# Performance work log

Hardware: AMD Instinct MI355X
Metric: run time of the kernel (lower is better)

Reference implementation:

```python
import jax, jax.numpy as jnp
from jax import lax
import numpy as np

B, FH, FW = 8, 50, 50
STRIDE = 16
SCALES = (8, 16, 32)
RATIOS = (0.5, 1.0, 2.0)
A = len(SCALES) * len(RATIOS)           # 9 anchors per location
G = 20                                   # gt boxes per image
IMG = FW * STRIDE                        # 800
PRE_NMS, POST_NMS, NMS_THR = 2000, 300, 0.7
POS_THR, NEG_THR = 0.7, 0.3
N_SAMPLES, POS_FRAC = 256, 0.5
SIGMA2 = 9.0                             # smooth-L1 sigma^2


def _make_anchors():
    # replicates ProposalLayer._generate_anchors (anchor-type-major ordering)
    xyp = np.arange(STRIDE / 2, FW * STRIDE, STRIDE).astype(int)
    centres = np.array(np.meshgrid(xyp, xyp)).T.reshape(-1, 2).astype(np.float32)
    dims = [[STRIDE * s * np.sqrt(r), STRIDE * s * np.sqrt(1.0 / r)]
            for s in SCALES for r in RATIOS]
    anc = np.concatenate([np.concatenate([centres - 0.5 * np.asarray(d, np.float32),
                                          centres + 0.5 * np.asarray(d, np.float32)], axis=1)
                          for d in dims], axis=0)
    inside = ((anc[:, 0] >= 0) & (anc[:, 1] >= 0) &
              (anc[:, 2] <= FH * STRIDE) & (anc[:, 3] <= FW * STRIDE))
    return anc, np.nonzero(inside)[0]

ANCHORS_NP, INSIDE_IDX = _make_anchors()
N_ANCH = ANCHORS_NP.shape[0]             # 22500 = FH*FW*A


def centrehw(b):
    return jnp.concatenate([(b[..., :2] + b[..., 2:]) * 0.5, b[..., 2:] - b[..., :2]], -1)

def yxcord(b):
    return jnp.concatenate([b[..., :2] - 0.5 * b[..., 2:], b[..., :2] + 0.5 * b[..., 2:]], -1)

def invtargets(d, a):
    return jnp.concatenate([a[..., :2] + d[..., :2] * a[..., 2:],
                            a[..., 2:] * jnp.exp(d[..., 2:])], -1)

def box_targets(g, a):
    return jnp.concatenate([(g[..., :2] - a[..., :2]) / a[..., 2:],
                            jnp.log(g[..., 2:] / a[..., 2:])], -1)

def pairwise_iou(b1, b2):
    # b1 [..., M, 4], b2 [..., N, 4] -> [..., M, N]
    a = b1[..., :, None, :]
    b = b2[..., None, :, :]
    tl = jnp.maximum(a[..., :2], b[..., :2])
    br = jnp.minimum(a[..., 2:], b[..., 2:])
    wh = jnp.clip(br - tl, 0.0)
    inter = wh[..., 0] * wh[..., 1]
    a1 = (a[..., 2] - a[..., 0]) * (a[..., 3] - a[..., 1])
    a2 = (b[..., 2] - b[..., 0]) * (b[..., 3] - b[..., 1])
    return inter / jnp.maximum(a1 + a2 - inter, 1e-8)


def _nms_single(boxes, scores):
    # greedy NMS: pre-NMS top-k, pairwise IoU, sequential suppression
    vals, idx = lax.top_k(scores, PRE_NMS)
    b = boxes[idx]                                 # [PRE, 4] score-descending
    iou = pairwise_iou(b, b)                       # [PRE, PRE]
    ar = jnp.arange(PRE_NMS)

    def step(supp, i):
        supp = supp | ((~supp[i]) & (iou[i] > NMS_THR) & (ar > i))
        return supp, None

    supp, _ = lax.scan(step, jnp.zeros(PRE_NMS, bool), jnp.arange(PRE_NMS))
    kv = jnp.where(supp, -jnp.inf, vals)
    tv, ti = lax.top_k(kv, POST_NMS)
    return b[ti] * jnp.isfinite(tv)[:, None]       # zero-pad if < POST kept


def _randsample(labels, key):
    # deterministic stand-in for torch randperm-based anchor subsampling
    r = jax.random.uniform(key, labels.shape)

    def ranks(mask):
        return jnp.argsort(jnp.argsort(jnp.where(mask, r, 2.0), axis=1), axis=1)

    pos = labels == 1
    neg = labels == 0
    n_pos = jnp.minimum(pos.sum(1), int(N_SAMPLES * POS_FRAC))
    keep_pos = pos & (ranks(pos) < n_pos[:, None])
    n_neg = jnp.minimum(neg.sum(1), N_SAMPLES - n_pos)
    keep_neg = neg & (ranks(neg) < n_neg[:, None])
    return jnp.where(keep_pos, 1, jnp.where(keep_neg, 0, -1)).astype(jnp.int32)


def _forward(pred_boxes, cls_scores, gt_boxes):
    anchors = jnp.asarray(ANCHORS_NP)
    ctrhw_a = centrehw(anchors)                    # [N, 4] (cy, cx, h, w)
    Bn = pred_boxes.shape[0]
    pd = pred_boxes.transpose(0, 2, 3, 1).reshape(Bn, -1, 4)     # [B, N, 4]
    cls2 = cls_scores.transpose(0, 2, 3, 1).reshape(Bn, -1, 2)   # [B, N, 2]
    pos_scores = cls_scores[:, A:].transpose(0, 2, 3, 1).reshape(Bn, -1)

    proposals = jnp.clip(yxcord(invtargets(pd, ctrhw_a[None])), 0.0, IMG - 1.0)
    top = jnp.floor(jax.vmap(_nms_single)(proposals, pos_scores))

    # ---- training losses ----
    iou = pairwise_iou(gt_boxes, anchors[None])    # [B, G, N]
    max_iou = iou.max(axis=1)
    argmax_bbox = jnp.argmax(iou, axis=1)          # best gt per anchor [B, N]
    labels = jnp.full((Bn, N_ANCH), -1, jnp.int32)
    labels = jnp.where(max_iou < NEG_THR, 0, labels)
    labels = jnp.where(max_iou >= POS_THR, 1, labels)
    gt_best = jnp.argmax(iou, axis=2)              # best anchor per gt [B, G]
    labels = labels.at[jnp.arange(Bn)[:, None], gt_best].set(1)
    labels = labels.at[:, INSIDE_IDX].set(-1)      # replicates source exactly as written
    labels = _randsample(labels, jax.random.key(42))

    g = jnp.take_along_axis(gt_boxes, argmax_bbox[:, :, None], axis=1)  # [B, N, 4]
    tgt = box_targets(centrehw(g), ctrhw_a[None])

    mask = labels != -1
    logp = jax.nn.log_softmax(cls2, axis=-1)
    per = -jnp.take_along_axis(logp, jnp.clip(labels, 0, 1)[..., None], axis=-1)[..., 0]
    cls_loss = (per * mask).sum() / jnp.maximum(mask.sum(), 1)

    in_w = (labels == 1).astype(pd.dtype)[..., None]
    out_w = mask.astype(pd.dtype)[..., None] / jnp.maximum((labels[0] >= 0).sum(), 1).astype(pd.dtype)
    d = in_w * (pd - tgt)
    ad = jnp.abs(d)
    l1 = jnp.where(ad < 1.0 / SIGMA2, 0.5 * SIGMA2 * d * d, ad - 0.5 / SIGMA2)
    bbox_loss = (out_w * l1).sum()
    return top, bbox_loss, cls_loss


def setup_inputs():
    key = jax.random.key(0)
    k1, k2, k3, k4 = jax.random.split(key, 4)
    pred_boxes = 0.1 * jax.random.normal(k1, (B, 4 * A, FH, FW), jnp.float32)
    cls_scores = jax.random.normal(k2, (B, 2 * A, FH, FW), jnp.float32)
    tl = jax.random.uniform(k3, (B, G, 2), minval=0.0, maxval=600.0)
    sz = jax.random.uniform(k4, (B, G, 2), minval=16.0, maxval=180.0)
    gt_boxes = jnp.concatenate([tl, jnp.minimum(tl + sz, IMG - 1.0)], axis=-1)
    return {"pred_boxes": pred_boxes, "cls_scores": cls_scores, "gt_boxes": gt_boxes}


def reference(pred_boxes, cls_scores, gt_boxes):
    return _forward(pred_boxes, cls_scores, gt_boxes)
```

## Files before the change

### kernel.cpp

```cpp
#include <hip/hip_runtime.h>
#include <math.h>

typedef unsigned long long u64;
typedef unsigned int u32;

#define BN 8
#define NA_T 9
#define NPOS 2500
#define FHW 50
#define N_ANCH 22500
#define NG 20
#define PRE 2000
#define POST 300
#define TOTAL (BN * N_ANCH)
#define HALF_RNG 90000u
#define NBLK 256
#define NFLAGS 240
#define MAGIC 0x9E3779B97F4A7C15ull

#define SCOPE_AGENT __HIP_MEMORY_SCOPE_AGENT


__device__ __forceinline__ float iou_f(float ax1, float ay1, float ax2, float ay2,
                                       float bx1, float by1, float bx2, float by2) {
    float tlx = fmaxf(ax1, bx1), tly = fmaxf(ay1, by1);
    float brx = fminf(ax2, bx2), bry = fminf(ay2, by2);
    float wx = fmaxf(brx - tlx, 0.0f);
    float wy = fmaxf(bry - tly, 0.0f);
    float inter = wx * wy;
    float a1 = (ax2 - ax1) * (ay2 - ay1);
    float a2 = (bx2 - bx1) * (by2 - by1);
    float den = fmaxf(a1 + a2 - inter, 1e-8f);
    return inter / den;
}

__device__ __forceinline__ unsigned int f32_sort_asc(float f) {
    unsigned int u = __float_as_uint(f);
    return (u & 0x80000000u) ? ~u : (u | 0x80000000u);
}

#define TF_R(r) { x0 += x1; x1 = ((x1 << r) | (x1 >> (32 - r))); x1 ^= x0; }
__device__ __forceinline__ unsigned int threefry_bits(unsigned int j) {
    unsigned int i = (j < HALF_RNG) ? j : j - HALF_RNG;
    unsigned int x0 = i, x1 = i + HALF_RNG;
    const unsigned int ks0 = 0u, ks1 = 42u, ks2 = 0x1BD11BDAu ^ 0u ^ 42u;
    x0 += ks0; x1 += ks1;
    TF_R(13) TF_R(15) TF_R(26) TF_R(6)
    x0 += ks1; x1 += ks2 + 1u;
    TF_R(17) TF_R(29) TF_R(16) TF_R(24)
    x0 += ks2; x1 += ks0 + 2u;
    TF_R(13) TF_R(15) TF_R(26) TF_R(6)
    x0 += ks0; x1 += ks1 + 3u;
    TF_R(17) TF_R(29) TF_R(16) TF_R(24)
    x0 += ks1; x1 += ks2 + 4u;
    TF_R(13) TF_R(15) TF_R(26) TF_R(6)
    x0 += ks2; x1 += ks0 + 5u;
    return (j < HALF_RNG) ? x0 : x1;
}

__device__ __forceinline__ float smooth_l1(float d) {
    float ad = fabsf(d);
    return (ad < (float)(1.0 / 9.0)) ? (4.5f * d) * d : (ad - (float)(0.5 / 9.0));
}

__device__ __forceinline__ u64 shflx64(u64 v, int m) {
    u32 lo = (u32)v, hi = (u32)(v >> 32);
    lo = (u32)__shfl_xor((int)lo, m);
    hi = (u32)__shfl_xor((int)hi, m);
    return (((u64)hi) << 32) | lo;
}

__device__ __forceinline__ u64 aload_rlx(u64* p) {
    return __hip_atomic_load(p, __ATOMIC_RELAXED, SCOPE_AGENT);
}
__device__ __forceinline__ void astore_rlx(u64* p, u64 v) {
    __hip_atomic_store(p, v, __ATOMIC_RELAXED, SCOPE_AGENT);
}
__device__ __forceinline__ void astore_u32(u32* p, u32 v) {
    __hip_atomic_store(p, v, __ATOMIC_RELAXED, SCOPE_AGENT);
}
__device__ __forceinline__ int aload32(int* p) {
    return __hip_atomic_load(p, __ATOMIC_RELAXED, SCOPE_AGENT);
}
__device__ __forceinline__ void astore32(int* p, int v) {
    __hip_atomic_store(p, v, __ATOMIC_RELAXED, SCOPE_AGENT);
}


struct Shm {
    u32 histA[4096];
    u64 poolB[2048];
    u64 sk[2048];
    float4 accb[POST];
    float accbA[POST];
    u64 Smat[64];
    u64 wsup[16];
    u32 s_out[2];
    u32 s_cnt, s_cnt2, s_cnt3;
    int s_scount;
    int sgb[NG];
    u64 sT, sTp, sTn;
    float2 whl[9];
    float4 g2[2 * NG];
    float swv[16];
    int swi[16];
    double rdc[32];
};

__device__ __forceinline__ void init_whl(Shm& S) {
    if (threadIdx.x < 9) {
        const double scl[3] = {8.0, 16.0, 32.0};
        const double rat[3] = {0.5, 1.0, 2.0};
        double s = 16.0 * scl[threadIdx.x / 3];
        double r = rat[threadIdx.x % 3];
        S.whl[threadIdx.x] = make_float2((float)(s * sqrt(r)), (float)(s * sqrt(1.0 / r)));
    }
}

__device__ __forceinline__ u64 block_sum_u64(u64 v, u64* sred, int nwaves) {
    for (int o = 32; o >= 1; o >>= 1) v += __shfl_down(v, o);
    int wid = threadIdx.x >> 6;
    if ((threadIdx.x & 63) == 0) sred[wid] = v;
    __syncthreads();
    u64 s = 0;
    for (int i = 0; i < nwaves; ++i) s += sred[i];
    return s;
}

__device__ __forceinline__ void hist_pick(const u32* hist, int nb,
                                          u32 remaining, u32* s_out) {
    if (threadIdx.x < 64) {
        int lane = threadIdx.x;
        int bpl = nb >> 6;
        int base = lane * bpl;
        u32 s = 0;
        for (int i = 0; i < bpl; ++i) s += hist[base + i];
        u32 p = s;
        for (int o = 1; o < 64; o <<= 1) {
            u32 t = __shfl_up(p, o);
            if (lane >= o) p += t;
        }
        u32 e = p - s;
        if (e < remaining && remaining <= p) {
            u32 cum = e;
            for (int i = 0; i < bpl; ++i) {
                u32 h = hist[base + i];
                if (cum + h >= remaining) {
                    s_out[0] = (u32)(base + i);
                    s_out[1] = remaining - cum;
                    break;
                }
                cum += h;
            }
        }
    }
    __syncthreads();
}

__device__ __forceinline__ int wave_push(u32* ctr, bool pred) {
    u64 m = __ballot(pred);
    if (m == 0) return -1;
    int lane = threadIdx.x & 63;
    int leader = __ffsll((long long)m) - 1;
    u32 base = 0;
    if (lane == leader) base = atomicAdd(ctr, (u32)__popcll(m));
    base = (u32)__shfl((int)base, leader);
    return pred ? (int)(base + __popcll(m & ((1ull << lane) - 1ull))) : -1;
}


__device__ __forceinline__ void topk_nms(Shm& S, const float* cls, const float* pred,
                                         float* out, int b) {
    int tid = threadIdx.x, lane = tid & 63, wid = tid >> 6;
    const float* cb = cls + ((size_t)b * 18 + 9) * NPOS;
    u32* skw = (u32*)S.sk;
    if (tid < 2) S.s_out[tid] = 0;
    for (int i = tid; i < 4096; i += 1024) { S.histA[i] = 0; skw[i] = 0; }
    __syncthreads();
    {
        int cpy = wid & 3;
        u32* H = ((cpy & 2) ? skw : S.histA) + ((cpy & 1) ? 2048 : 0);
        u32 xr = (u32)(cpy << 3);
        for (int i = tid; i < 5625; i += 1024) {
            float4 v = ((const float4*)cb)[i];
            atomicAdd(&H[(((~f32_sort_asc(v.x)) >> 21) ^ xr)], 1u);
            atomicAdd(&H[(((~f32_sort_asc(v.y)) >> 21) ^ xr)], 1u);
            atomicAdd(&H[(((~f32_sort_asc(v.z)) >> 21) ^ xr)], 1u);
            atomicAdd(&H[(((~f32_sort_asc(v.w)) >> 21) ^ xr)], 1u);
        }
    }
    __syncthreads();
    for (int bn = tid; bn < 2048; bn += 1024) {
        u32 s0 = S.histA[bn];
        u32 s1 = S.histA[2048 + (bn ^ 8)];
        u32 s2 = skw[bn ^ 16];
        u32 s3 = skw[2048 + (bn ^ 24)];
        S.histA[bn] = s0 + s1 + s2 + s3;
    }
    __syncthreads();
    hist_pick(S.histA, 2048, PRE, S.s_out);
    u32 d0 = S.s_out[0], r0 = S.s_out[1];
    u32 bincnt = S.histA[d0];
    bool fast = bincnt <= 2048;
    for (int i = tid; i < 2048; i += 1024) S.sk[i] = 0xFFFFFFFFFFFFFFFFull - (u32)i;
    if (tid == 0) { S.s_cnt = 0; S.s_cnt2 = 0; }
    __syncthreads();
    for (int c = 0; c < 22; ++c) {
        int m = tid + c * 1024;
        bool valid = m < N_ANCH;
        u32 kd = valid ? ~f32_sort_asc(cb[m]) : 0xFFFFFFFFu;
        int n = valid ? ((m % NPOS) * 9 + m / NPOS) : 0;
        u64 kk = (((u64)kd) << 15) | (u32)n;
        u32 topb = kd >> 21;
        int ps = wave_push(&S.s_cnt, valid && topb < d0);
        if (ps >= 0) S.sk[ps] = kk;
        int pb = wave_push(&S.s_cnt2, valid && fast && topb == d0);
        if (pb >= 0) S.poolB[pb] = kk;
    }
    __syncthreads();
    int bc = (int)S.s_cnt2;

    u64 T;
    u64 prefix = ((u64)d0) << 36;
    if (fast) {
        for (int i = tid; i < 4096; i += 1024) S.histA[i] = 0;
        __syncthreads();
        u64 himask = ~((1ull << 36) - 1);
        for (int i = tid; i < bc; i += 1024) {
            u64 kk = S.poolB[i];
            if ((kk & himask) == prefix)
                atomicAdd(&S.histA[(u32)((kk >> 24) & 4095ull)], 1u);
        }
        __syncthreads();
        hist_pick(S.histA, 4096, r0, S.s_out);
        u64 prefix2 = prefix | (((u64)S.s_out[0]) << 24);
        u32 rem2 = S.s_out[1];
        __syncthreads();
        u64* subb = (u64*)S.histA;
        if (tid == 0) S.s_cnt3 = 0;
        __syncthreads();
        u64 himask2 = ~((1ull << 24) - 1);
        for (int i = tid; i < bc; i += 1024) {
            u64 kk = S.poolB[i];
            int ps = wave_push(&S.s_cnt3, (kk & himask2) == prefix2);
            if (ps >= 0) subb[ps] = kk;
        }
        __syncthreads();
        int sc = (int)S.s_cnt3;
        for (int i = tid; i < sc; i += 1024) {
            u64 ki = subb[i]; int rank = 0;
            for (int j = 0; j < sc; ++j) rank += (subb[j] < ki);
            if (rank == (int)rem2 - 1) S.sT = ki;
        }
        __syncthreads();
        T = S.sT;
        for (int i = tid; i < bc; i += 1024) {
            u64 kk = S.poolB[i];
            int ps = wave_push(&S.s_cnt, kk <= T);
            if (ps >= 0) S.sk[ps] = kk;
        }
    } else {
        u32 remaining = r0;
        for (int p = 0; p < 3; ++p) {
            int sh = 24 - 12 * p;
            for (int i = tid; i < 4096; i += 1024) S.histA[i] = 0;
            __syncthreads();
            u64 himask = ~((1ull << (sh + 12)) - 1);
            for (int c = 0; c < 22; ++c) {
                int m = tid + c * 1024;
                if (m < N_ANCH) {
                    int n = (m % NPOS) * 9 + m / NPOS;
                    u64 kk = (((u64)(~f32_sort_asc(cb[m]))) << 15) | (u32)n;
                    if ((kk & himask) == prefix)
                        atomicAdd(&S.histA[(u32)((kk >> sh) & 4095ull)], 1u);
                }
            }
            __syncthreads();
            hist_pick(S.histA, 4096, remaining, S.s_out);
            prefix |= ((u64)S.s_out[0]) << sh;
            remaining = S.s_out[1];
            __syncthreads();
        }
        T = prefix;
        for (int c = 0; c < 22; ++c) {
            int m = tid + c * 1024;
            bool valid = m < N_ANCH;
            u32 kd = valid ? ~f32_sort_asc(cb[m]) : 0xFFFFFFFFu;
            int n = valid ? ((m % NPOS) * 9 + m / NPOS) : 0;
            u64 kk = (((u64)kd) << 15) | (u32)n;
            int ps = wave_push(&S.s_cnt, valid && (kd >> 21) == d0 && kk <= T);
            if (ps >= 0) S.sk[ps] = kk;
        }
    }
    __syncthreads();

    {
        int base = wid * 128;
        u64 v0 = S.sk[base + lane];
        u64 v1 = S.sk[base + 64 + lane];
        for (int k = 2; k <= 128; k <<= 1) {
            bool up0 = ((lane & k) == 0);
            bool up1 = (((64 + lane) & k) == 0);
            for (int j = k >> 1; j > 0; j >>= 1) {
                if (j == 64) {
                    u64 lo = v0 < v1 ? v0 : v1;
                    u64 hi = v0 < v1 ? v1 : v0;
                    v0 = lo; v1 = hi;
                } else {
                    u64 p0 = shflx64(v0, j);
                    u64 p1 = shflx64(v1, j);
                    bool lower = ((lane & j) == 0);
                    bool km0 = (lower == up0);
                    bool km1 = (lower == up1);
                    v0 = km0 ? (v0 < p0 ? v0 : p0) : (v0 > p0 ? v0 : p0);
                    v1 = km1 ? (v1 < p1 ? v1 : p1) : (v1 > p1 ? v1 : p1);
                }
            }
        }
        S.sk[base + lane] = v0;
        S.sk[base + 64 + lane] = v1;
    }
    __syncthreads();

    {
        u64* src = S.sk; u64* dst = S.poolB;
        for (int Sz = 128; Sz < 2048; Sz <<= 1) {
            for (int e = 0; e < 2; ++e) {
                int i = tid + e * 1024;
                u64 key = src[i];
                int pairBase = i & ~(2 * Sz - 1);
                int t = i - pairBase;
                const u64* other; int p;
                if (t < Sz) { other = src + pairBase + Sz; p = t; }
                else        { other = src + pairBase;      p = t - Sz; }
                int lo = 0, hi = Sz;
                while (lo < hi) {
                    int mid = (lo + hi) >> 1;
                    if (other[mid] < key) lo = mid + 1; else hi = mid;
                }
                dst[pairBase + p + lo] = key;
            }
            __syncthreads();
            u64* tmp = src; src = dst; dst = tmp;
        }
    }

    float2* bl = (float2*)S.poolB;
    float2* bh = (float2*)S.sk;
    for (int i = tid; i < 2048; i += 1024) {
        float2 lo = make_float2(0.f, 0.f), hi = make_float2(0.f, 0.f);
        if (i < PRE) {
            int n = (int)(S.sk[i] & 0x7fffu);
            int d = n / NPOS, k = n % NPOS;
            float2 wh = S.whl[d];
            float cx = (float)(8 + 16 * (k / FHW));
            float cy = (float)(8 + 16 * (k % FHW));
            float ax1 = cx - 0.5f * wh.x, ay1 = cy - 0.5f * wh.y;
            float ax2 = cx + 0.5f * wh.x, ay2 = cy + 0.5f * wh.y;
            float acx = (ax1 + ax2) * 0.5f, acy = (ay1 + ay2) * 0.5f;
            float aw = ax2 - ax1, ah = ay2 - ay1;
            int a = n % NA_T, hw = n / NA_T;
            const float* pb = pred + (size_t)b * 36 * NPOS;
            float dx = pb[(4 * a + 0) * NPOS + hw];
            float dy = pb[(4 * a + 1) * NPOS + hw];
            float dw = pb[(4 * a + 2) * NPOS + hw];
            float dh = pb[(4 * a + 3) * NPOS + hw];
            float px = acx + dx * aw, py = acy + dy * ah;
            float pw = aw * expf(dw), ph = ah * expf(dh);
            float x1 = px - 0.5f * pw, y1 = py - 0.5f * ph;
            float x2 = px + 0.5f * pw, y2 = py + 0.5f * ph;
            x1 = fminf(fmaxf(x1, 0.0f), 799.0f);
            y1 = fminf(fmaxf(y1, 0.0f), 799.0f);
            x2 = fminf(fmaxf(x2, 0.0f), 799.0f);
            y2 = fminf(fmaxf(y2, 0.0f), 799.0f);
            lo = make_float2(x1, y1); hi = make_float2(x2, y2);
        }
        bl[i] = lo; bh[i] = hi;
    }
    if (tid == 0) S.s_scount = 0;
    __syncthreads();

    for (int c = 0; c < 32; ++c) {
        int A = S.s_scount;
        int base = c * 64;
        float2 clo = bl[base + lane], chi = bh[base + lane];
        float myA = (chi.x - clo.x) * (chi.y - clo.y);
        bool sup = false;
        for (int a = wid; a < A; a += 16) {
            float4 ab = S.accb[a];
            float tlx = fmaxf(ab.x, clo.x), tly = fmaxf(ab.y, clo.y);
            float brx = fminf(ab.z, chi.x), bry = fminf(ab.w, chi.y);
            float wx = fmaxf(brx - tlx, 0.0f), wy = fmaxf(bry - tly, 0.0f);
            float inter = wx * wy;
            float den = fmaxf(S.accbA[a] + myA - inter, 1e-8f);
            sup |= inter > 0.7f * den;
            if (__all(sup)) break;
        }
        u64 bal = __ballot(sup);
        if (lane == 0) S.wsup[wid] = bal;
        #pragma unroll
        for (int q = 0; q < 4; ++q) {
            int o = wid * 4 + q;
            float2 olo = bl[base + o], ohi = bh[base + o];
            float oA = (ohi.x - olo.x) * (ohi.y - olo.y);
            float tlx = fmaxf(olo.x, clo.x), tly = fmaxf(olo.y, clo.y);
            float brx = fminf(ohi.x, chi.x), bry = fminf(ohi.y, chi.y);
            float wx = fmaxf(brx - tlx, 0.0f), wy = fmaxf(bry - tly, 0.0f);
            float inter = wx * wy;
            float den = fmaxf(oA + myA - inter, 1e-8f);
            bool hit = inter > 0.7f * den;
            u64 m = __ballot(hit);
            if (lane == 0) S.Smat[o] = m;
        }
        __syncthreads();
        if (wid == 0) {
            u64 my_smat = S.Smat[lane];
            u32 sm_lo = (u32)my_smat, sm_hi = (u32)(my_smat >> 32);
            u64 supmask = 0;
            #pragma unroll
            for (int i2 = 0; i2 < 16; ++i2) supmask |= S.wsup[i2];
            int jmax = min(64, PRE - base);
            u64 valid = (jmax >= 64) ? ~0ull : ((1ull << jmax) - 1ull);
            u64 live = (~supmask) & valid;
            int count = A;
            u64 accmask = 0;
            while (live && count < POST) {
                int i = __ffsll((long long)live) - 1;
                u32 rlo = (u32)__builtin_amdgcn_readlane((int)sm_lo, i);
                u32 rhi = (u32)__builtin_amdgcn_readlane((int)sm_hi, i);
                u64 sm = (((u64)rhi) << 32) | rlo;
                accmask |= (1ull << i);
                live &= ~sm & ~(1ull << i);
                count++;
            }
            if (accmask & (1ull << lane)) {
                int pos = A + __popcll(accmask & ((1ull << lane) - 1ull));
                S.accb[pos] = make_float4(clo.x, clo.y, chi.x, chi.y);
                S.accbA[pos] = myA;
            }
            if (lane == 0) S.s_scount = count;
        }
        __syncthreads();
        if (S.s_scount >= POST) break;
    }
    int cntk = S.s_scount;
    for (int s = tid; s < POST; s += 1024) {
        float4 v = make_float4(0.f, 0.f, 0.f, 0.f);
        if (s < cntk) {
            float4 p = S.accb[s];
            v = make_float4(floorf(p.x), floorf(p.y), floorf(p.z), floorf(p.w));
        }
        ((float4*)out)[(size_t)b * POST + s] = v;
    }
}


__device__ __forceinline__ void sample_loss(Shm& S, const u32* samp, int* gtb,
                                            const float* pred, const float* cls,
                                            const float* gt, u64* slots, int b) {
    int tid = threadIdx.x, lane = tid & 63, wid = tid >> 6;
    u32* bitmap = (u32*)S.poolB;
    u64* sred   = S.poolB + 512;
    u64* bufN   = S.poolB + 640;
    u32* hP = S.histA;
    u32* hN = S.histA + 2048;
    u64* bufP = S.sk;
    u64* bufNf = S.sk + 1024;
    const u32* sb = samp + (size_t)b * N_ANCH;

    if (tid < 2) S.s_out[tid] = 0;
    for (int i = tid; i < 704; i += 1024) bitmap[i] = 0;
    for (int i = tid; i < 4096; i += 1024) S.histA[i] = 0;
    if (tid < NG) S.sgb[tid] = aload32(&gtb[b * NG + tid]);
    __syncthreads();

    for (int i = tid; i < 5625; i += 1024) {
        uint4 v = ((const uint4*)sb)[i];
        #pragma unroll
        for (int q = 0; q < 4; ++q) {
            u32 sp = (q == 0) ? v.x : (q == 1) ? v.y : (q == 2) ? v.z : v.w;
            int enc = (int)(sp & 3u);
            if (enc == 2) atomicAdd(&hP[sp >> 21], 1u);
            if (enc == 1) atomicAdd(&hN[sp >> 21], 1u);
        }
    }
    if (tid < NG) {
        int gn = S.sgb[tid];
        atomicOr(&bitmap[gn >> 5], 1u << (gn & 31));
    }
    __syncthreads();
    if (tid < NG) {
        int gn = S.sgb[tid];
        bool dup = false;
        for (int j = 0; j < tid; ++j) dup |= (S.sgb[j] == gn);
        if (!dup) {
            u32 sp = sb[(gn % 9) * NPOS + gn / 9];
            int enc = (int)(sp & 3u);
            if (enc != 3) {
                if (enc != 2) atomicAdd(&hP[sp >> 21], 1u);
                if (enc == 1) atomicSub(&hN[sp >> 21], 1u);
            }
        }
    }
    __syncthreads();

    u32 aP = 0, aN = 0;
    for (int i = tid; i < 2048; i += 1024) { aP += hP[i]; aN += hN[i]; }
    u64 packed = block_sum_u64(((u64)aP << 32) | (u64)aN, sred, 16);
    int cpt = (int)(packed >> 32), ctot = (int)(packed & 0xffffffffu);
    int np = min(cpt, 128), nn = min(ctot, 256 - np);

    bool needP = cpt > np, needN = ctot > nn;
    u32 dN = 0, remN = 0;
    if (needN) {
        hist_pick(hN, 2048, (u32)nn, S.s_out);
        dN = S.s_out[0]; remN = S.s_out[1];
        __syncthreads();
    }
    int gN = needN ? (nn - (int)remN + (int)hN[dN]) : ctot;
    bool fastS = (cpt <= 2048) && (gN <= 512);

    if (tid == 0) { S.s_cnt = 0; S.s_cnt2 = 0; }
    __syncthreads();

    double lcls = 0.0, lbox = 0.0;

    if (fastS) {
        for (int c = 0; c < 22; ++c) {
            int m = tid + c * 1024;
            bool valid = m < N_ANCH;
            u32 sp = valid ? sb[m] : 0u;
            int enc = (int)(sp & 3u);
            int n = valid ? ((m % NPOS) * 9 + m / NPOS) : 0;
            bool bm = valid && ((bitmap[n >> 5] >> (n & 31)) & 1u);
            int l = (enc == 3) ? -1 : (bm ? 1 : enc - 1);
            u64 kk = (((u64)(sp >> 9)) << 15) | (u32)n;
            int pp = wave_push(&S.s_cnt, valid && l == 1);
            if (pp >= 0) bufP[pp] = kk;
            int pn = wave_push(&S.s_cnt2, valid && l == 0 && (!needN || (sp >> 21) <= dN));
            if (pn >= 0) bufN[pn] = kk;
        }
        __syncthreads();
        int cntP = (int)S.s_cnt;
        int cntN = (int)S.s_cnt2;

        if (needP) {
            for (int i = tid; i < cntP; i += 1024) {
                u64 ki = bufP[i]; int rank = 0;
                for (int j = 0; j < cntP; ++j) rank += (bufP[j] < ki);
                if (rank == np - 1) S.sTp = ki;
            }
        }
        if (needN) {
            for (int i = tid; i < cntN; i += 1024) {
                u64 ki = bufN[i]; int rank = 0;
                for (int j = 0; j < cntN; ++j) rank += (bufN[j] < ki);
                if (rank == nn - 1) S.sTn = ki;
            }
        }
        __syncthreads();
        u64 Tp = needP ? S.sTp : ~0ull;
        u64 Tn = needN ? S.sTn : ~0ull;

        for (int i = tid; i < cntP; i += 1024) {
            u64 kk = bufP[i];
            if (kk > Tp) continue;
            int n = (int)(kk & 0x7fffu);
            int a = n % NA_T, hw = n / NA_T;
            int m = a * NPOS + hw;
            float l0 = cls[((size_t)b * 18 + 2 * a + 0) * NPOS + hw];
            float l1 = cls[((size_t)b * 18 + 2 * a + 1) * NPOS + hw];
            float mx = fmaxf(l0, l1);
            float s0 = l0 - mx, s1 = l1 - mx;
            float lse = logf(expf(s0) + expf(s1));
            lcls += (double)(-(s1 - lse));
            u32 sp = sb[m];
            const float* pb = pred + (size_t)b * 36 * NPOS;
            float dx = pb[(4 * a + 0) * NPOS + hw];
            float dy = pb[(4 * a + 1) * NPOS + hw];
            float dw = pb[(4 * a + 2) * NPOS + hw];
            float dh = pb[(4 * a + 3) * NPOS + hw];
            int d = n / NPOS, k = n % NPOS;
            float2 wh = S.whl[d];
            float cx = (float)(8 + 16 * (k / FHW));
            float cy = (float)(8 + 16 * (k % FHW));
            float ax1 = cx - 0.5f * wh.x, ay1 = cy - 0.5f * wh.y;
            float ax2 = cx + 0.5f * wh.x, ay2 = cy + 0.5f * wh.y;
            float acx = (ax1 + ax2) * 0.5f, acy = (ay1 + ay2) * 0.5f;
            float aw = ax2 - ax1, ah = ay2 - ay1;
            float4 G = ((const float4*)gt)[b * NG + ((sp >> 4) & 31u)];
            float gcx = (G.x + G.z) * 0.5f, gcy = (G.y + G.w) * 0.5f;
            float gw = G.z - G.x, gh = G.w - G.y;
            float t0 = (gcx - acx) / aw, t1 = (gcy - acy) / ah;
            float t2 = logf(gw / aw), t3 = logf(gh / ah);
            lbox += (double)(smooth_l1(dx - t0) + smooth_l1(dy - t1) +
                             smooth_l1(dw - t2) + smooth_l1(dh - t3));
        }
        for (int i = tid; i < cntN; i += 1024) {
            u64 kk = bufN[i];
            if (kk > Tn) continue;
            int n = (int)(kk & 0x7fffu);
            int a = n % NA_T, hw = n / NA_T;
            float l0 = cls[((size_t)b * 18 + 2 * a + 0) * NPOS + hw];
            float l1 = cls[((size_t)b * 18 + 2 * a + 1) * NPOS + hw];
            float mx = fmaxf(l0, l1);
            float s0 = l0 - mx, s1 = l1 - mx;
            float lse = logf(expf(s0) + expf(s1));
            lcls += (double)(-(s0 - lse));
        }
    } else {
        u32 dP = 0, remP = 0;
        if (needP) {
            hist_pick(hP, 2048, (u32)np, S.s_out);
            dP = S.s_out[0]; remP = S.s_out[1];
            __syncthreads();
        }
        for (int c = 0; c < 22; ++c) {
            int m = tid + c * 1024;
            bool valid = m < N_ANCH;
            u32 sp = valid ? sb[m] : 0u;
            int enc = (int)(sp & 3u);
            int n = valid ? ((m % NPOS) * 9 + m / NPOS) : 0;
            bool bm = valid && ((bitmap[n >> 5] >> (n & 31)) & 1u);
            int l = (enc == 3) ? -1 : (bm ? 1 : enc - 1);
            u64 kk = (((u64)(sp >> 9)) << 15) | (u32)n;
            int pp = wave_push(&S.s_cnt, valid && needP && l == 1 && (sp >> 21) == dP);
            if (pp >= 0 && pp < 1024) bufP[pp] = kk;
            int pn = wave_push(&S.s_cnt2, valid && needN && l == 0 && (sp >> 21) == dN);
            if (pn >= 0 && pn < 1024) bufNf[pn] = kk;
        }
        __syncthreads();
        if (needP) {
            int cnt = min((int)S.s_cnt, 1024);
            for (int i = tid; i < cnt; i += 1024) {
                u64 ki = bufP[i]; int rank = 0;
                for (int j = 0; j < cnt; ++j) rank += (bufP[j] < ki);
                if (rank == (int)remP - 1) S.sTp = ki;
            }
        }
        if (needN) {
            int cnt = min((int)S.s_cnt2, 1024);
            for (int i = tid; i < cnt; i += 1024) {
                u64 ki = bufNf[i]; int rank = 0;
                for (int j = 0; j < cnt; ++j) rank += (bufNf[j] < ki);
                if (rank == (int)remN - 1) S.sTn = ki;
            }
        }
        __syncthreads();
        u64 Tp = needP ? S.sTp : ~0ull;
        u64 Tn = needN ? S.sTn : ~0ull;

        for (int c = 0; c < 22; ++c) {
            int m = tid + c * 1024;
            if (m >= N_ANCH) continue;
            u32 sp = sb[m];
            int enc = (int)(sp & 3u);
            int n = (m % NPOS) * 9 + m / NPOS;
            bool bm = (bitmap[n >> 5] >> (n & 31)) & 1u;
            int l = (enc == 3) ? -1 : (bm ? 1 : enc - 1);
            if (l < 0) continue;
            u64 kk = (((u64)(sp >> 9)) << 15) | (u32)n;
            int lab = -1;
            if (l == 1) { if (kk <= Tp) lab = 1; }
            else        { if (kk <= Tn) lab = 0; }
            if (lab < 0) continue;
            int a = m / NPOS, hw = m % NPOS;
            float l0 = cls[((size_t)b * 18 + 2 * a + 0) * NPOS + hw];
            float l1 = cls[((size_t)b * 18 + 2 * a + 1) * NPOS + hw];
            float mx = fmaxf(l0, l1);
            float s0 = l0 - mx, s1 = l1 - mx;
            float lse = logf(expf(s0) + expf(s1));
            lcls += (double)(-((lab ? s1 : s0) - lse));
            if (lab == 1) {
                const float* pb = pred + (size_t)b * 36 * NPOS;
                float dx = pb[(4 * a + 0) * NPOS + hw];
                float dy = pb[(4 * a + 1) * NPOS + hw];
                float dw = pb[(4 * a + 2) * NPOS + hw];
                float dh = pb[(4 * a + 3) * NPOS + hw];
                int d = n / NPOS, k = n % NPOS;
                float2 wh = S.whl[d];
                float cx = (float)(8 + 16 * (k / FHW));
                float cy = (float)(8 + 16 * (k % FHW));
                float ax1 = cx - 0.5f * wh.x, ay1 = cy - 0.5f * wh.y;
                float ax2 = cx + 0.5f * wh.x, ay2 = cy + 0.5f * wh.y;
                float acx = (ax1 + ax2) * 0.5f, acy = (ay1 + ay2) * 0.5f;
                float aw = ax2 - ax1, ah = ay2 - ay1;
                float4 G = ((const float4*)gt)[b * NG + ((sp >> 4) & 31u)];
                float gcx = (G.x + G.z) * 0.5f, gcy = (G.y + G.w) * 0.5f;
                float gw = G.z - G.x, gh = G.w - G.y;
                float t0 = (gcx - acx) / aw, t1 = (gcy - acy) / ah;
                float t2 = logf(gw / aw), t3 = logf(gh / ah);
                lbox += (double)(smooth_l1(dx - t0) + smooth_l1(dy - t1) +
                                 smooth_l1(dw - t2) + smooth_l1(dh - t3));
            }
        }
    }

    for (int o = 32; o >= 1; o >>= 1) {
        lcls += __shfl_down(lcls, o);
        lbox += __shfl_down(lbox, o);
    }
    if (lane == 0) { S.rdc[wid] = lcls; S.rdc[16 + wid] = lbox; }
    __syncthreads();
    if (tid == 0) {
        double A = 0.0, Bv = 0.0;
        for (int i = 0; i < 16; ++i) { A += S.rdc[i]; Bv += S.rdc[16 + i]; }
        astore_rlx(&slots[b * 4 + 0], (u64)__double_as_longlong(A));
        astore_rlx(&slots[b * 4 + 1], (u64)__double_as_longlong(Bv));
        astore_rlx(&slots[b * 4 + 2], (u64)(np + nn));
        asm volatile("s_waitcnt vmcnt(0)" ::: "memory");
        astore_rlx(&slots[b * 4 + 3], MAGIC);
    }
}


__global__ void __launch_bounds__(1024) k_all(const float* __restrict__ pred,
    const float* __restrict__ cls, const float* __restrict__ gt, float* __restrict__ out,
    u32* __restrict__ samp, int* __restrict__ gtb,
    u64* __restrict__ slots, u64* __restrict__ flags)
{
    __shared__ Shm S;
    int tid = threadIdx.x, bid = blockIdx.x;
    int lane = tid & 63, wid = tid >> 6;
    init_whl(S);

    if (bid < BN) {
        __syncthreads();
        topk_nms(S, cls, pred, out, bid);
        if (bid == 0 && tid == 0) {
            for (int bb = 0; bb < BN; ++bb)
                while (aload_rlx(&slots[bb * 4 + 3]) != MAGIC) __builtin_amdgcn_s_sleep(2);
            double a0 = 0.0, a1 = 0.0; int total = 0, c0 = 0;
            for (int bb = 0; bb < BN; ++bb) {
                a0 += __longlong_as_double((long long)aload_rlx(&slots[bb * 4 + 0]));
                a1 += __longlong_as_double((long long)aload_rlx(&slots[bb * 4 + 1]));
                int v = (int)aload_rlx(&slots[bb * 4 + 2]);
                total += v;
                if (bb == 0) c0 = v;
            }
            out[BN * POST * 4 + 0] = (float)(a1 / (double)max(c0, 1));
            out[BN * POST * 4 + 1] = (float)(a0 / (double)max(total, 1));
        }
        return;
    }

    if (bid < 2 * BN) {
        if (tid < NFLAGS) {
            while (aload_rlx(&flags[tid]) != MAGIC) __builtin_amdgcn_s_sleep(2);
        }
        __syncthreads();
        __builtin_amdgcn_fence(__ATOMIC_ACQUIRE, "agent");
        __syncthreads();
        sample_loss(S, samp, gtb, pred, cls, gt, slots, bid - BN);
        return;
    }

    if (bid < 192) {
        int g0 = (bid - 16) * 1024;
        int b0 = g0 / N_ANCH;
        int b1 = (g0 + 1023) / N_ANCH; if (b1 >= BN) b1 = BN - 1;
        if (tid < NG) S.g2[tid] = ((const float4*)gt)[b0 * NG + tid];
        if (b1 > b0 && tid >= NG && tid < 2 * NG)
            S.g2[tid] = ((const float4*)gt)[b1 * NG + (tid - NG)];
        __syncthreads();
        int g = g0 + tid;
        if (g < TOTAL) {
            int b = g / N_ANCH, m = g % N_ANCH;
            int a = m / NPOS, hw = m % NPOS;
            int n = hw * 9 + a;
            int d = n / NPOS, k = n % NPOS;
            float2 wh = S.whl[d];
            float cx = (float)(8 + 16 * (k / FHW));
            float cy = (float)(8 + 16 * (k % FHW));
            float ax1 = cx - 0.5f * wh.x, ay1 = cy - 0.5f * wh.y;
            float ax2 = cx + 0.5f * wh.x, ay2 = cy + 0.5f * wh.y;
            const float4* gg = &S.g2[(b == b0) ? 0 : NG];
            float best = -1.0f; int bi = 0;
            for (int gi = 0; gi < NG; ++gi) {
                float4 G = gg[gi];
                float v = iou_f(G.x, G.y, G.z, G.w, ax1, ay1, ax2, ay2);
                if (v > best) { best = v; bi = gi; }
            }
            int lab = -1;
            if (best < 0.3f) lab = 0;
            if (best >= 0.7f) lab = 1;
            bool inside = (ax1 >= 0.0f && ay1 >= 0.0f && ax2 <= 800.0f && ay2 <= 800.0f);
            int enc = inside ? 3 : (lab + 1);
            u32 mant = threefry_bits((u32)(b * N_ANCH + n)) >> 9;
            astore_u32(&samp[g], (mant << 9) | ((u32)bi << 4) | (u32)enc);
        }
    } else {
        int j = bid - 192;
        int ntask = (j < 32) ? 3 : 2;
        for (int q = 0; q < ntask; ++q) {
            int gid = (q < 2) ? (j * 2 + q) : (128 + j);
            int b = gid / NG, gi = gid % NG;
            float4 G = ((const float4*)gt)[b * NG + gi];
            float best = -1.0f; int bidx = N_ANCH;
            for (int d = 0; d < 9; ++d) {
                float2 wh = S.whl[d];
                for (int k = tid; k < NPOS; k += 1024) {
                    float cx = (float)(8 + 16 * (k / FHW));
                    float cy = (float)(8 + 16 * (k % FHW));
                    float x1 = cx - 0.5f * wh.x, y1 = cy - 0.5f * wh.y;
                    float x2 = cx + 0.5f * wh.x, y2 = cy + 0.5f * wh.y;
                    float v = iou_f(G.x, G.y, G.z, G.w, x1, y1, x2, y2);
                    if (v > best) { best = v; bidx = d * NPOS + k; }
                }
            }
            for (int o = 1; o < 64; o <<= 1) {
                float v2 = __shfl_xor(best, o); int i2 = __shfl_xor(bidx, o);
                if (v2 > best || (v2 == best && i2 < bidx)) { best = v2; bidx = i2; }
            }
            if (lane == 0) { S.swv[wid] = best; S.swi[wid] = bidx; }
            __syncthreads();
            if (wid == 0) {
                float bv = (lane < 16) ? S.swv[lane] : -1.0f;
                int bx = (lane < 16) ? S.swi[lane] : N_ANCH;
                for (int o = 1; o < 16; o <<= 1) {
                    float v2 = __shfl_xor(bv, o); int i2 = __shfl_xor(bx, o);
                    if (v2 > bv || (v2 == bv && i2 < bx)) { bv = v2; bx = i2; }
                }
                if (lane == 0) astore32(&gtb[gid], bx);
            }
            __syncthreads();
        }
    }
    __syncthreads();
    if (tid == 0) astore_rlx(&flags[bid - 16], MAGIC);
}


extern "C" void kernel_launch(void* const* d_in, const int* in_sizes, int n_in,
                              void* d_out, int out_size, void* d_ws, size_t ws_size,
                              hipStream_t stream) {
    (void)in_sizes; (void)n_in; (void)out_size; (void)ws_size;
    const float* pred = (const float*)d_in[0];
    const float* cls  = (const float*)d_in[1];
    const float* gt   = (const float*)d_in[2];
    float* out = (float*)d_out;

    char* w = (char*)d_ws;
    size_t off = 0;
    auto take = [&](size_t bytes) { void* p = w + off; off += (bytes + 255) & ~(size_t)255; return p; };
    u64* flags = (u64*)take((size_t)NFLAGS * 8);
    u64* slots = (u64*)take((size_t)BN * 4 * 8);
    u32* samp  = (u32*)take((size_t)TOTAL * 4);
    int* gtb   = (int*)take(160 * 4);

    hipLaunchKernelGGL(k_all, dim3(NBLK), dim3(1024), 0, stream,
                       pred, cls, gt, out, samp, gtb, slots, flags);
}
```

Measured before the change: 137.1 us.

## Split top-k histogram and candidate compaction across four helper blocks per image

Blocks 16–47 now each take a quarter of one image's foreground scores. Each builds a partial radix histogram, publishes it to global memory, waits for its three siblings, picks the threshold bin, and compacts the above-threshold and boundary-bin keys into per-quarter global buffers. The per-image NMS blocks wait on these flags, sum the four histograms, gather the compacted keys and go straight to the back half of top-k. If the counts fail a consistency check, they fall back to the full single-block path. This moves the serial 22.5K-element scan off the critical NMS blocks. The cost is extra spin-wait flag handshakes, global round trips, and added work on helper blocks that also feed the sample/loss stage.

```diff
diff --git a/kernel.cpp b/kernel.cpp
--- a/kernel.cpp
+++ b/kernel.cpp
@@ -105,6 +105,7 @@
     float swv[16];
     int swi[16];
     double rdc[32];
+    u32 hcnt[194];
 };
 
 __device__ __forceinline__ void init_whl(Shm& S) {
@@ -169,55 +170,9 @@
 }
 
 
-__device__ __forceinline__ void topk_nms(Shm& S, const float* cls, const float* pred,
-                                         float* out, int b) {
+__device__ void topk_back(Shm& S, const float* cb, const float* pred, float* out, int b,
+                          u32 d0, u32 r0, u32 bincnt, bool fast) {
     int tid = threadIdx.x, lane = tid & 63, wid = tid >> 6;
-    const float* cb = cls + ((size_t)b * 18 + 9) * NPOS;
-    u32* skw = (u32*)S.sk;
-    if (tid < 2) S.s_out[tid] = 0;
-    for (int i = tid; i < 4096; i += 1024) { S.histA[i] = 0; skw[i] = 0; }
-    __syncthreads();
-    {
-        int cpy = wid & 3;
-        u32* H = ((cpy & 2) ? skw : S.histA) + ((cpy & 1) ? 2048 : 0);
-        u32 xr = (u32)(cpy << 3);
-        for (int i = tid; i < 5625; i += 1024) {
-            float4 v = ((const float4*)cb)[i];
-            atomicAdd(&H[(((~f32_sort_asc(v.x)) >> 21) ^ xr)], 1u);
-            atomicAdd(&H[(((~f32_sort_asc(v.y)) >> 21) ^ xr)], 1u);
-            atomicAdd(&H[(((~f32_sort_asc(v.z)) >> 21) ^ xr)], 1u);
-            atomicAdd(&H[(((~f32_sort_asc(v.w)) >> 21) ^ xr)], 1u);
-        }
-    }
-    __syncthreads();
-    for (int bn = tid; bn < 2048; bn += 1024) {
-        u32 s0 = S.histA[bn];
-        u32 s1 = S.histA[2048 + (bn ^ 8)];
-        u32 s2 = skw[bn ^ 16];
-        u32 s3 = skw[2048 + (bn ^ 24)];
-        S.histA[bn] = s0 + s1 + s2 + s3;
-    }
-    __syncthreads();
-    hist_pick(S.histA, 2048, PRE, S.s_out);
-    u32 d0 = S.s_out[0], r0 = S.s_out[1];
-    u32 bincnt = S.histA[d0];
-    bool fast = bincnt <= 2048;
-    for (int i = tid; i < 2048; i += 1024) S.sk[i] = 0xFFFFFFFFFFFFFFFFull - (u32)i;
-    if (tid == 0) { S.s_cnt = 0; S.s_cnt2 = 0; }
-    __syncthreads();
-    for (int c = 0; c < 22; ++c) {
-        int m = tid + c * 1024;
-        bool valid = m < N_ANCH;
-        u32 kd = valid ? ~f32_sort_asc(cb[m]) : 0xFFFFFFFFu;
-        int n = valid ? ((m % NPOS) * 9 + m / NPOS) : 0;
-        u64 kk = (((u64)kd) << 15) | (u32)n;
-        u32 topb = kd >> 21;
-        int ps = wave_push(&S.s_cnt, valid && topb < d0);
-        if (ps >= 0) S.sk[ps] = kk;
-        int pb = wave_push(&S.s_cnt2, valid && fast && topb == d0);
-        if (pb >= 0) S.poolB[pb] = kk;
-    }
-    __syncthreads();
     int bc = (int)S.s_cnt2;
 
     u64 T;
@@ -452,6 +407,58 @@
         }
         ((float4*)out)[(size_t)b * POST + s] = v;
     }
+}
+
+
+__device__ void topk_full(Shm& S, const float* cls, const float* pred, float* out, int b) {
+    int tid = threadIdx.x, wid = tid >> 6;
+    const float* cb = cls + ((size_t)b * 18 + 9) * NPOS;
+    u32* skw = (u32*)S.sk;
+    if (tid < 2) S.s_out[tid] = 0;
+    for (int i = tid; i < 4096; i += 1024) { S.histA[i] = 0; skw[i] = 0; }
+    __syncthreads();
+    {
+        int cpy = wid & 3;
+        u32* H = ((cpy & 2) ? skw : S.histA) + ((cpy & 1) ? 2048 : 0);
+        u32 xr = (u32)(cpy << 3);
+        for (int i = tid; i < 5625; i += 1024) {
+            float4 v = ((const float4*)cb)[i];
+            atomicAdd(&H[(((~f32_sort_asc(v.x)) >> 21) ^ xr)], 1u);
+            atomicAdd(&H[(((~f32_sort_asc(v.y)) >> 21) ^ xr)], 1u);
+            atomicAdd(&H[(((~f32_sort_asc(v.z)) >> 21) ^ xr)], 1u);
+            atomicAdd(&H[(((~f32_sort_asc(v.w)) >> 21) ^ xr)], 1u);
+        }
+    }
+    __syncthreads();
+    for (int bn = tid; bn < 2048; bn += 1024) {
+        u32 s0 = S.histA[bn];
+        u32 s1 = S.histA[2048 + (bn ^ 8)];
+        u32 s2 = skw[bn ^ 16];
+        u32 s3 = skw[2048 + (bn ^ 24)];
+        S.histA[bn] = s0 + s1 + s2 + s3;
+    }
+    __syncthreads();
+    hist_pick(S.histA, 2048, PRE, S.s_out);
+    u32 d0 = S.s_out[0], r0 = S.s_out[1];
+    u32 bincnt = S.histA[d0];
+    bool fast = bincnt <= 2048;
+    for (int i = tid; i < 2048; i += 1024) S.sk[i] = 0xFFFFFFFFFFFFFFFFull - (u32)i;
+    if (tid == 0) { S.s_cnt = 0; S.s_cnt2 = 0; }
+    __syncthreads();
+    for (int c = 0; c < 22; ++c) {
+        int m = tid + c * 1024;
+        bool valid = m < N_ANCH;
+        u32 kd = valid ? ~f32_sort_asc(cb[m]) : 0xFFFFFFFFu;
+        int n = valid ? ((m % NPOS) * 9 + m / NPOS) : 0;
+        u64 kk = (((u64)kd) << 15) | (u32)n;
+        u32 topb = kd >> 21;
+        int ps = wave_push(&S.s_cnt, valid && topb < d0);
+        if (ps >= 0) S.sk[ps] = kk;
+        int pb = wave_push(&S.s_cnt2, valid && fast && topb == d0);
+        if (pb >= 0) S.poolB[pb] = kk;
+    }
+    __syncthreads();
+    topk_back(S, cb, pred, out, b, d0, r0, bincnt, fast);
 }
 
 
@@ -717,7 +724,9 @@
 __global__ void __launch_bounds__(1024) k_all(const float* __restrict__ pred,
     const float* __restrict__ cls, const float* __restrict__ gt, float* __restrict__ out,
     u32* __restrict__ samp, int* __restrict__ gtb,
-    u64* __restrict__ slots, u64* __restrict__ flags)
+    u64* __restrict__ slots, u64* __restrict__ flags,
+    u64* __restrict__ hflag, u64* __restrict__ cflag, u64* __restrict__ cnt64,
+    u32* __restrict__ histreg, u64* __restrict__ blwreg, u64* __restrict__ binreg)
 {
     __shared__ Shm S;
     int tid = threadIdx.x, bid = blockIdx.x;
@@ -725,8 +734,60 @@
     init_whl(S);
 
     if (bid < BN) {
-        __syncthreads();
-        topk_nms(S, cls, pred, out, bid);
+        int b = bid;
+        const float* cb = cls + ((size_t)b * 18 + 9) * NPOS;
+        for (int i = tid; i < 2048; i += 1024) S.sk[i] = 0xFFFFFFFFFFFFFFFFull - (u32)i;
+        if (tid < 2) S.s_out[tid] = 0;
+        if (tid < 4) {
+            while (aload_rlx(&cflag[b * 4 + tid]) != MAGIC) __builtin_amdgcn_s_sleep(2);
+        }
+        __syncthreads();
+        __builtin_amdgcn_fence(__ATOMIC_ACQUIRE, "agent");
+        __syncthreads();
+        if (tid < 4) {
+            u64 cc = cnt64[b * 4 + tid];
+            S.sgb[tid] = (int)(cc >> 32);
+            S.sgb[4 + tid] = (int)(cc & 0xffffffffu);
+        }
+        const u32* hr = histreg + (size_t)b * 4 * 2048;
+        for (int i = tid; i < 2048; i += 1024)
+            S.histA[i] = hr[i] + hr[2048 + i] + hr[4096 + i] + hr[6144 + i];
+        __syncthreads();
+        hist_pick(S.histA, 2048, PRE, S.s_out);
+        u32 d0 = S.s_out[0], r0 = S.s_out[1];
+        u32 bincnt = S.histA[d0];
+        bool fast = bincnt <= 2048;
+        int tb[4], tx[4];
+        bool bounds = true;
+        int tBsum = 0, tXsum = 0;
+        for (int r = 0; r < 4; ++r) {
+            tb[r] = S.sgb[r]; tx[r] = S.sgb[4 + r];
+            bounds = bounds && tb[r] >= 0 && tb[r] <= 2047 && tx[r] >= 0 && tx[r] <= 2048;
+            tBsum += tb[r]; tXsum += tx[r];
+        }
+        bool ok = fast && bounds && tBsum == (int)(PRE - r0) && tXsum == (int)bincnt;
+        __syncthreads();
+        if (ok) {
+            const u64* blw = blwreg + (size_t)b * 4 * 2048;
+            const u64* bnr = binreg + (size_t)b * 4 * 2048;
+            int off = 0;
+            for (int r = 0; r < 4; ++r) {
+                int c = tb[r];
+                for (int i = tid; i < c; i += 1024) S.sk[off + i] = blw[r * 2048 + i];
+                off += c;
+            }
+            off = 0;
+            for (int r = 0; r < 4; ++r) {
+                int c = tx[r];
+                for (int i = tid; i < c; i += 1024) S.poolB[off + i] = bnr[r * 2048 + i];
+                off += c;
+            }
+            if (tid == 0) { S.s_cnt = (u32)tBsum; S.s_cnt2 = (u32)tXsum; }
+            __syncthreads();
+            topk_back(S, cb, pred, out, b, d0, r0, bincnt, fast);
+        } else {
+            topk_full(S, cls, pred, out, b);
+        }
         if (bid == 0 && tid == 0) {
             for (int bb = 0; bb < BN; ++bb)
                 while (aload_rlx(&slots[bb * 4 + 3]) != MAGIC) __builtin_amdgcn_s_sleep(2);
@@ -753,6 +814,102 @@
         __syncthreads();
         sample_loss(S, samp, gtb, pred, cls, gt, slots, bid - BN);
         return;
+    }
+
+    if (bid < 48) {
+        int hb = (bid - 16) >> 2, hq = (bid - 16) & 3;
+        const float* cb = cls + ((size_t)hb * 18 + 9) * NPOS;
+        int mlo = hq * 5632, mhi = min(N_ANCH, mlo + 5632);
+        u32* skw = (u32*)S.sk;
+        for (int i = tid; i < 4096; i += 1024) { S.histA[i] = 0; skw[i] = 0; }
+        __syncthreads();
+        {
+            int cpy = wid & 3;
+            u32* H = ((cpy & 2) ? skw : S.histA) + ((cpy & 1) ? 2048 : 0);
+            u32 xr = (u32)(cpy << 3);
+            int vlo = mlo >> 2, vhi = mhi >> 2;
+            for (int i = vlo + tid; i < vhi; i += 1024) {
+                float4 v = ((const float4*)cb)[i];
+                atomicAdd(&H[(((~f32_sort_asc(v.x)) >> 21) ^ xr)], 1u);
+                atomicAdd(&H[(((~f32_sort_asc(v.y)) >> 21) ^ xr)], 1u);
+                atomicAdd(&H[(((~f32_sort_asc(v.z)) >> 21) ^ xr)], 1u);
+                atomicAdd(&H[(((~f32_sort_asc(v.w)) >> 21) ^ xr)], 1u);
+            }
+        }
+        __syncthreads();
+        for (int bn = tid; bn < 2048; bn += 1024) {
+            u32 s0 = S.histA[bn];
+            u32 s1 = S.histA[2048 + (bn ^ 8)];
+            u32 s2 = skw[bn ^ 16];
+            u32 s3 = skw[2048 + (bn ^ 24)];
+            S.histA[bn] = s0 + s1 + s2 + s3;
+        }
+        __syncthreads();
+        u32* myh = histreg + (size_t)(hb * 4 + hq) * 2048;
+        for (int i = tid; i < 2048; i += 1024) astore_u32(&myh[i], S.histA[i]);
+        __syncthreads();
+        if (tid == 0) astore_rlx(&hflag[hb * 4 + hq], MAGIC);
+        if (tid < 4) {
+            while (aload_rlx(&hflag[hb * 4 + tid]) != MAGIC) __builtin_amdgcn_s_sleep(2);
+        }
+        __syncthreads();
+        __builtin_amdgcn_fence(__ATOMIC_ACQUIRE, "agent");
+        __syncthreads();
+        const u32* hr = histreg + (size_t)hb * 4 * 2048;
+        for (int i = tid; i < 2048; i += 1024)
+            S.histA[i] = hr[i] + hr[2048 + i] + hr[4096 + i] + hr[6144 + i];
+        if (tid < 2) S.s_out[tid] = 0;
+        __syncthreads();
+        hist_pick(S.histA, 2048, PRE, S.s_out);
+        u32 d0 = S.s_out[0];
+        u32 bincnt = S.histA[d0];
+        bool fast = bincnt <= 2048;
+        u32 kdreg[6];
+        for (int c = 0; c < 6; ++c) {
+            int m = mlo + tid + c * 1024;
+            bool valid = m < mhi;
+            u32 kd = valid ? ~f32_sort_asc(cb[m]) : 0xFFFFFFFFu;
+            kdreg[c] = kd;
+            u32 topb = kd >> 21;
+            u64 bb = __ballot(valid && topb < d0);
+            u64 bx = __ballot(valid && fast && topb == d0);
+            if (lane == 0) {
+                S.hcnt[c * 16 + wid] = (u32)__popcll(bb);
+                S.hcnt[96 + c * 16 + wid] = (u32)__popcll(bx);
+            }
+        }
+        __syncthreads();
+        if (tid == 0) {
+            u32 s = 0;
+            for (int i = 0; i < 96; ++i) { u32 t = S.hcnt[i]; S.hcnt[i] = s; s += t; }
+            S.hcnt[192] = s;
+            s = 0;
+            for (int i = 96; i < 192; ++i) { u32 t = S.hcnt[i]; S.hcnt[i] = s; s += t; }
+            S.hcnt[193] = s;
+        }
+        __syncthreads();
+        u64* myblw = blwreg + (size_t)(hb * 4 + hq) * 2048;
+        u64* mybin = binreg + (size_t)(hb * 4 + hq) * 2048;
+        u64 lmask = (1ull << lane) - 1ull;
+        for (int c = 0; c < 6; ++c) {
+            int m = mlo + tid + c * 1024;
+            bool valid = m < mhi;
+            u32 kd = kdreg[c];
+            u32 topb = kd >> 21;
+            bool isb = valid && topb < d0;
+            bool isx = valid && fast && topb == d0;
+            u64 bb = __ballot(isb);
+            u64 bx = __ballot(isx);
+            int n = valid ? ((m % NPOS) * 9 + m / NPOS) : 0;
+            u64 kk = (((u64)kd) << 15) | (u32)n;
+            if (isb) astore_rlx(&myblw[S.hcnt[c * 16 + wid] + __popcll(bb & lmask)], kk);
+            if (isx) astore_rlx(&mybin[S.hcnt[96 + c * 16 + wid] + __popcll(bx & lmask)], kk);
+        }
+        __syncthreads();
+        if (tid == 0)
+            astore_rlx(&cnt64[hb * 4 + hq], (((u64)S.hcnt[192]) << 32) | (u64)S.hcnt[193]);
+        __syncthreads();
+        if (tid == 0) astore_rlx(&cflag[hb * 4 + hq], MAGIC);
     }
 
     if (bid < 192) {
@@ -843,11 +1000,18 @@
     char* w = (char*)d_ws;
     size_t off = 0;
     auto take = [&](size_t bytes) { void* p = w + off; off += (bytes + 255) & ~(size_t)255; return p; };
-    u64* flags = (u64*)take((size_t)NFLAGS * 8);
-    u64* slots = (u64*)take((size_t)BN * 4 * 8);
-    u32* samp  = (u32*)take((size_t)TOTAL * 4);
-    int* gtb   = (int*)take(160 * 4);
+    u64* flags   = (u64*)take((size_t)NFLAGS * 8);
+    u64* hflag   = (u64*)take((size_t)32 * 8);
+    u64* cflag   = (u64*)take((size_t)32 * 8);
+    u64* slots   = (u64*)take((size_t)BN * 4 * 8);
+    u64* cnt64   = (u64*)take((size_t)32 * 8);
+    u32* histreg = (u32*)take((size_t)8 * 4 * 2048 * 4);
+    u64* blwreg  = (u64*)take((size_t)8 * 4 * 2048 * 8);
+    u64* binreg  = (u64*)take((size_t)8 * 4 * 2048 * 8);
+    u32* samp    = (u32*)take((size_t)TOTAL * 4);
+    int* gtb     = (int*)take(160 * 4);
 
     hipLaunchKernelGGL(k_all, dim3(NBLK), dim3(1024), 0, stream,
-                       pred, cls, gt, out, samp, gtb, slots, flags);
-}
+                       pred, cls, gt, out, samp, gtb, slots, flags,
+                       hflag, cflag, cnt64, histreg, blwreg, binreg);
+}
```

Measured after the change: 149.2 us. 8.8% more time.
